# Kernel tuning notes

Measured on AMD Instinct MI355X. Metric: run time of the kernel, lower is better.

The kernel has to match this reference:

```python
import jax, jax.numpy as jnp
import numpy as np

N_NODES = 100000
N_EDGES = 1600000
IN_F, HID_F, OUT_F = 128, 128, 64


def setup_inputs() -> dict:
    key = jax.random.key(0)
    ks = jax.random.split(key, 8)
    x = jax.random.normal(ks[0], (N_NODES, IN_F), dtype=jnp.float32)
    edge_index = jax.random.randint(ks[1], (2, N_EDGES), 0, N_NODES, dtype=jnp.int64)
    w1 = jax.random.normal(ks[2], (IN_F, HID_F), dtype=jnp.float32) * 0.05
    b1 = jax.random.normal(ks[3], (HID_F,), dtype=jnp.float32) * 0.05
    c1 = jax.random.normal(ks[4], (IN_F, HID_F, 3), dtype=jnp.float32) * 0.01
    w2 = jax.random.normal(ks[5], (HID_F, OUT_F), dtype=jnp.float32) * 0.05
    b2 = jax.random.normal(ks[6], (OUT_F,), dtype=jnp.float32) * 0.05
    c2 = jax.random.normal(ks[7], (IN_F, OUT_F, 3), dtype=jnp.float32) * 0.01
    return {"x": x, "edge_index": edge_index, "w1": w1, "b1": b1, "c1": c1,
            "w2": w2, "b2": b2, "c2": c2}


def _minimal_kan(x, w, b, c):
    # linear term: (N, out)
    lin = x @ w + b
    # polynomial basis (x, x^2, x^3): (N, in, 3)
    basis = jnp.stack([x, x * x, x * x * x], axis=-1)
    # fused contraction over (in, 3); same math as the (N,in,out,3) broadcast-sum
    kan_out = jnp.einsum('nib,iob->no', basis, c)
    return lin + 0.1 * kan_out


def _aggregate(h, source, target, num_nodes):
    # mean over incoming messages, degree clamped at 1
    deg = jax.ops.segment_sum(jnp.ones(source.shape[0], dtype=h.dtype), target,
                              num_segments=num_nodes)
    deg = jnp.maximum(deg, 1.0)
    out = jax.ops.segment_sum(h[source], target, num_segments=num_nodes)
    return out / deg[:, None]


def reference(x, edge_index, w1, b1, c1, w2, b2, c2):
    source, target = edge_index[0], edge_index[1]
    n = x.shape[0]
    h = _minimal_kan(x, w1, b1, c1)
    h = jax.nn.relu(h)
    h = _aggregate(h, source, target, n)
    h = _minimal_kan(h, w2, b2, c2)
    h = _aggregate(h, source, target, n)
    return jax.nn.log_softmax(h, axis=-1)
```

## Files before the change

kernel.cpp:

```cpp
#include <hip/hip_runtime.h>
#include <hip/hip_bf16.h>
#include <math.h>

#define N_NODES 100000
#define N_EDGES 1600000
#define IN_F 128
#define HID_F 128
#define OUT_F 64
#define K_TOT 384
#define BST 392

#define BK_BITS 9
#define BK_SIZE 512
#define NBUCK ((N_NODES + BK_SIZE - 1) / BK_SIZE)
#define EPB 4096
#define NBLK_SORT ((N_EDGES + EPB - 1) / EPB)
#define BCAP 10240
#define PK_SRC_MASK 0x7fffffu
#define PAD8(d) (((d) + 7) & ~7)

typedef __attribute__((ext_vector_type(8))) short s8v;
typedef __attribute__((ext_vector_type(4))) short s4v;
typedef __attribute__((ext_vector_type(4))) float f4v;
typedef __attribute__((ext_vector_type(2))) float f2v;

__device__ __forceinline__ short f2bf(float f) {
    __hip_bfloat16 h = __float2bfloat16(f);
    return __builtin_bit_cast(short, h);
}

__global__ __launch_bounds__(256) void fold_weights_bf16(
    const float* __restrict__ w1, const float* __restrict__ c1,
    const float* __restrict__ w2, const float* __restrict__ c2,
    short* __restrict__ Wb1, short* __restrict__ Wb2,
    unsigned* __restrict__ h1d, unsigned* __restrict__ h2d)
{
    if (blockIdx.x == 0) {
        if (threadIdx.x < 32) h1d[(size_t)N_NODES * 32 + threadIdx.x] = 0;
        if (threadIdx.x < 16) h2d[(size_t)N_NODES * 16 + threadIdx.x] = 0;
    }
    int idx = blockIdx.x * 256 + threadIdx.x;
    if (idx < K_TOT * HID_F) {
        int k = idx >> 7, n = idx & 127;
        int p = k >> 7, f = k & 127;
        int si = f * HID_F + n;
        float v = (p == 0) ? (w1[si] + 0.1f * c1[si * 3])
                           : 0.1f * c1[si * 3 + p];
        Wb1[(((k >> 3) * HID_F) + n) * 8 + (k & 7)] = f2bf(v);
    } else {
        idx -= K_TOT * HID_F;
        if (idx < K_TOT * OUT_F) {
            int k = idx >> 6, n = idx & 63;
            int p = k >> 7, f = k & 127;
            int si = f * OUT_F + n;
            float v = (p == 0) ? (w2[si] + 0.1f * c2[si * 3])
                               : 0.1f * c2[si * 3 + p];
            Wb2[(((k >> 3) * OUT_F) + n) * 8 + (k & 7)] = f2bf(v);
        }
    }
}

__global__ __launch_bounds__(256) void bucket_init(int* __restrict__ bcur)
{
    int i = threadIdx.x;
    if (i < NBUCK) bcur[i] = i * BCAP;
}

__global__ __launch_bounds__(256) void bucket_scatter(
    const int* __restrict__ src, const int* __restrict__ tgt,
    int* __restrict__ bcur, unsigned* __restrict__ spk)
{
    __shared__ int h[NBUCK];
    __shared__ int base[NBUCK];
    int tid = threadIdx.x;
    for (int i = tid; i < NBUCK; i += 256) h[i] = 0;
    __syncthreads();
    int e0 = blockIdx.x * EPB;
    int n = min(EPB, N_EDGES - e0);
    for (int i = tid; i < n; i += 256)
        atomicAdd(&h[tgt[e0 + i] >> BK_BITS], 1);
    __syncthreads();
    for (int i = tid; i < NBUCK; i += 256) {
        int c = h[i];
        base[i] = c ? atomicAdd(&bcur[i], c) : 0;
        h[i] = 0;
    }
    __syncthreads();
    for (int i = tid; i < n; i += 256) {
        int t = tgt[e0 + i];
        int b = t >> BK_BITS;
        int pos = base[b] + atomicAdd(&h[b], 1);
        spk[pos] = ((unsigned)(t - (b << BK_BITS)) << 23) | (unsigned)src[e0 + i];
    }
}

__global__ __launch_bounds__(256) void bucket_degpad(
    const int* __restrict__ bcur, const unsigned* __restrict__ spk,
    int* __restrict__ deg, int* __restrict__ pbsum)
{
    __shared__ int d[BK_SIZE];
    __shared__ int s[256];
    int tid = threadIdx.x;
    int b = blockIdx.x;
    d[tid] = 0; d[tid + 256] = 0;
    __syncthreads();
    int e0 = b * BCAP, e1 = bcur[b];
    for (int i = e0 + tid; i < e1; i += 256)
        atomicAdd(&d[spk[i] >> 23], 1);
    __syncthreads();
    int nbase = b << BK_BITS;
    int a0 = d[2 * tid], a1c = d[2 * tid + 1];
    int n0 = nbase + 2 * tid, n1 = n0 + 1;
    if (n0 < N_NODES) deg[n0] = a0;
    if (n1 < N_NODES) deg[n1] = a1c;
    int pc0 = (n0 < N_NODES) ? PAD8(a0) : 0;
    int pc1 = (n1 < N_NODES) ? PAD8(a1c) : 0;
    s[tid] = pc0 + pc1;
    __syncthreads();
    for (int o = 128; o > 0; o >>= 1) {
        if (tid < o) s[tid] += s[tid + o];
        __syncthreads();
    }
    if (tid == 0) pbsum[b] = s[0];
}

__global__ __launch_bounds__(256) void csr_finalize(
    const int* __restrict__ bcur, const unsigned* __restrict__ spk,
    const int* __restrict__ deg, const int* __restrict__ pbsum,
    int* __restrict__ prow, int* __restrict__ csr_pad)
{
    __shared__ int s[256];
    __shared__ int cur[BK_SIZE];
    __shared__ int pst[BK_SIZE];
    int tid = threadIdx.x;
    int b = blockIdx.x;

    int v = (tid < NBUCK) ? pbsum[tid] : 0;
    s[tid] = v;
    __syncthreads();
    for (int o = 1; o < 256; o <<= 1) {
        int t = (tid >= o) ? s[tid - o] : 0;
        __syncthreads();
        s[tid] += t;
        __syncthreads();
    }
    int pboff_b = (b > 0) ? s[b - 1] : 0;
    int ptotal  = s[NBUCK - 1];
    __syncthreads();

    int nbase = b << BK_BITS;
    int n0 = nbase + 2 * tid, n1 = n0 + 1;
    int d0 = (n0 < N_NODES) ? deg[n0] : 0;
    int d1 = (n1 < N_NODES) ? deg[n1] : 0;
    int pc0 = (n0 < N_NODES) ? PAD8(d0) : 0;
    int pc1 = (n1 < N_NODES) ? PAD8(d1) : 0;
    int tsum = pc0 + pc1;
    s[tid] = tsum;
    __syncthreads();
    for (int o = 1; o < 256; o <<= 1) {
        int t = (tid >= o) ? s[tid - o] : 0;
        __syncthreads();
        s[tid] += t;
        __syncthreads();
    }
    int excl = s[tid] - tsum;
    int base = pboff_b + excl;
    if (n0 < N_NODES) { prow[n0] = base;       cur[2 * tid]     = base;       pst[2 * tid]     = base + pc0; }
    if (n1 < N_NODES) { prow[n1] = base + pc0; cur[2 * tid + 1] = base + pc0; pst[2 * tid + 1] = base + pc0 + pc1; }
    if (b == NBUCK - 1 && tid == 0) prow[N_NODES] = ptotal;
    __syncthreads();

    int e0 = b * BCAP, e1 = bcur[b];
    for (int i = e0 + tid; i < e1; i += 256) {
        unsigned pk = spk[i];
        int pos = atomicAdd(&cur[pk >> 23], 1);
        csr_pad[pos] = (int)(pk & PK_SRC_MASK);
    }
    __syncthreads();

    for (int i = tid; i < BK_SIZE; i += 256) {
        int nd = nbase + i;
        if (nd < N_NODES) {
            int kend = pst[i];
            for (int k = cur[i]; k < kend; ++k) csr_pad[k] = N_NODES;
        }
    }
}

__global__ __launch_bounds__(256) void kan1_mfma(
    const float* __restrict__ x, const short* __restrict__ Wb,
    const float* __restrict__ bias, unsigned* __restrict__ h1d)
{
    __shared__ short sb[64 * BST];
    const int tid  = threadIdx.x;
    const int lane = tid & 63;
    const int wave = tid >> 6;
    const int node0 = blockIdx.x * 64;
    const int q = lane >> 4, r = lane & 15;

#pragma unroll
    for (int it = 0; it < 8; ++it) {
        int idx = tid + 256 * it;
        int m = idx >> 5, c4 = (idx & 31) * 4;
        int gm = min(node0 + m, N_NODES - 1);
        float4 v = *(const float4*)(x + (size_t)gm * IN_F + c4);
        float vv[4] = {v.x, v.y, v.z, v.w};
        s4v p0, p1, p2;
#pragma unroll
        for (int t = 0; t < 4; ++t) {
            float e = vv[t], e2 = e * e, e3 = e2 * e;
            p0[t] = f2bf(e); p1[t] = f2bf(e2); p2[t] = f2bf(e3);
        }
        short* row = sb + m * BST + c4;
        *(s4v*)(row)       = p0;
        *(s4v*)(row + 128) = p1;
        *(s4v*)(row + 256) = p2;
    }
    __syncthreads();

    const int wm = (wave & 1) * 32;
    const int wn = (wave >> 1) * 64;

    f4v acc[2][4];
#pragma unroll
    for (int i = 0; i < 2; ++i)
#pragma unroll
        for (int j = 0; j < 4; ++j)
            acc[i][j] = (f4v){0.f, 0.f, 0.f, 0.f};

    float bj[4];
#pragma unroll
    for (int j = 0; j < 4; ++j) bj[j] = bias[wn + j * 16 + r];

#pragma unroll
    for (int kb = 0; kb < 12; ++kb) {
        const int col = kb * 32 + q * 8;
        s8v afrag[2];
#pragma unroll
        for (int i = 0; i < 2; ++i)
            afrag[i] = *(const s8v*)(sb + (wm + i * 16 + r) * BST + col);
#pragma unroll
        for (int j = 0; j < 4; ++j) {
            const s8v b = *(const s8v*)(Wb + (((kb * 4 + q) * HID_F) + wn + j * 16 + r) * 8);
            acc[0][j] = __builtin_amdgcn_mfma_f32_16x16x32_bf16(afrag[0], b, acc[0][j], 0, 0, 0);
            acc[1][j] = __builtin_amdgcn_mfma_f32_16x16x32_bf16(afrag[1], b, acc[1][j], 0, 0, 0);
        }
    }

    const int dci = ((wn >> 6) << 4) + r;
#pragma unroll
    for (int i = 0; i < 2; ++i)
#pragma unroll
        for (int e = 0; e < 4; ++e) {
            int grow = node0 + wm + i * 16 + q * 4 + e;
            if (grow < N_NODES) {
                float v0 = fmaxf(acc[i][0][e] + bj[0], 0.f);
                float v1 = fmaxf(acc[i][1][e] + bj[1], 0.f);
                float v2 = fmaxf(acc[i][2][e] + bj[2], 0.f);
                float v3 = fmaxf(acc[i][3][e] + bj[3], 0.f);
                int pk = __builtin_amdgcn_cvt_pk_fp8_f32(v0, v1, 0, false);
                pk = __builtin_amdgcn_cvt_pk_fp8_f32(v2, v3, pk, true);
                h1d[(size_t)grow * 32 + dci] = (unsigned)pk;
            }
        }
}

__global__ __launch_bounds__(256) void gather128(
    const unsigned* __restrict__ h1d, const int* __restrict__ prow,
    const int* __restrict__ csr_pad, unsigned* __restrict__ a1d)
{
    const int lane  = threadIdx.x & 63;
    const int wave  = threadIdx.x >> 6;
    const int hl    = lane & 31;
    const int half  = lane >> 5;
    const int hbase = half << 5;
    const int node  = blockIdx.x * 8 + wave * 2 + half;

    int p0 = prow[node], p1 = prow[node + 1];
    int cnt = p1 - p0;
    int cmax = max(cnt, __shfl_xor(cnt, 32));

    float acc[4][4];
#pragma unroll
    for (int t = 0; t < 4; ++t)
#pragma unroll
        for (int b = 0; b < 4; ++b) acc[t][b] = 0.f;

    for (int base = 0; base < cmax; base += 32) {
        int idx = max(min(p0 + base + hl, p1 - 1), 0);
        int sreg = csr_pad[idx];
        int lim = min(32, cmax - base);
        for (int j = 0; j < lim; j += 4) {
            if (base + j < cnt) {
                unsigned u[4];
#pragma unroll
                for (int t = 0; t < 4; ++t) {
                    int sj = __shfl(sreg, hbase + j + t);
                    u[t] = h1d[(size_t)sj * 32 + hl];
                }
#pragma unroll
                for (int t = 0; t < 4; ++t) {
                    f2v lo = __builtin_amdgcn_cvt_pk_f32_fp8(u[t], false);
                    f2v hi = __builtin_amdgcn_cvt_pk_f32_fp8(u[t], true);
                    acc[t][0] += lo.x; acc[t][1] += lo.y;
                    acc[t][2] += hi.x; acc[t][3] += hi.y;
                }
            }
        }
    }

    float s0 = (acc[0][0] + acc[1][0]) + (acc[2][0] + acc[3][0]);
    float s1 = (acc[0][1] + acc[1][1]) + (acc[2][1] + acc[3][1]);
    float s2 = (acc[0][2] + acc[1][2]) + (acc[2][2] + acc[3][2]);
    float s3 = (acc[0][3] + acc[1][3]) + (acc[2][3] + acc[3][3]);
    int pk = __builtin_amdgcn_cvt_pk_fp8_f32(s0, s1, 0, false);
    pk = __builtin_amdgcn_cvt_pk_fp8_f32(s2, s3, pk, true);
    a1d[(size_t)node * 32 + hl] = (unsigned)pk;
}

__global__ __launch_bounds__(256) void kan2_mfma(
    const unsigned* __restrict__ a1d, const int* __restrict__ deg,
    const short* __restrict__ Wb, const float* __restrict__ bias,
    unsigned short* __restrict__ h2s)
{
    __shared__ short sb[64 * BST];
    const int tid  = threadIdx.x;
    const int lane = tid & 63;
    const int wave = tid >> 6;
    const int node0 = blockIdx.x * 64;
    const int q = lane >> 4, r = lane & 15;

#pragma unroll
    for (int gi = 0; gi < 2; ++gi) {
        int g = tid + 256 * gi;
        int m = g >> 3, cg = (g & 7) * 4;
        int gm = min(node0 + m, N_NODES - 1);
        float di = 1.0f / fmaxf((float)deg[gm], 1.0f);
        uint4 u4 = *(const uint4*)(a1d + (size_t)gm * 32 + cg);
        unsigned uw[4] = {u4.x, u4.y, u4.z, u4.w};
        float xv[4][4];
#pragma unroll
        for (int j = 0; j < 4; ++j) {
            f2v lo = __builtin_amdgcn_cvt_pk_f32_fp8(uw[j], false);
            f2v hi = __builtin_amdgcn_cvt_pk_f32_fp8(uw[j], true);
            xv[j][0] = lo.x * di; xv[j][1] = lo.y * di;
            xv[j][2] = hi.x * di; xv[j][3] = hi.y * di;
        }
        int fb = ((cg >> 4) << 6) + (cg & 15);
#pragma unroll
        for (int b = 0; b < 4; ++b) {
            s4v p0, p1, p2;
#pragma unroll
            for (int j = 0; j < 4; ++j) {
                float e = xv[j][b], e2 = e * e, e3 = e2 * e;
                p0[j] = f2bf(e); p1[j] = f2bf(e2); p2[j] = f2bf(e3);
            }
            short* row = sb + m * BST + fb + 16 * b;
            *(s4v*)(row)       = p0;
            *(s4v*)(row + 128) = p1;
            *(s4v*)(row + 256) = p2;
        }
    }
    __syncthreads();

    const int wm = (wave & 1) * 32;
    const int wn = (wave >> 1) * 32;

    f4v acc[2][2];
#pragma unroll
    for (int i = 0; i < 2; ++i)
#pragma unroll
        for (int j = 0; j < 2; ++j)
            acc[i][j] = (f4v){0.f, 0.f, 0.f, 0.f};

    float bj[2];
#pragma unroll
    for (int j = 0; j < 2; ++j) bj[j] = bias[wn + j * 16 + r];

#pragma unroll
    for (int kb = 0; kb < 12; ++kb) {
        const int col = kb * 32 + q * 8;
        s8v afrag[2];
#pragma unroll
        for (int i = 0; i < 2; ++i)
            afrag[i] = *(const s8v*)(sb + (wm + i * 16 + r) * BST + col);
#pragma unroll
        for (int j = 0; j < 2; ++j) {
            const s8v b = *(const s8v*)(Wb + (((kb * 4 + q) * OUT_F) + wn + j * 16 + r) * 8);
            acc[0][j] = __builtin_amdgcn_mfma_f32_16x16x32_bf16(afrag[0], b, acc[0][j], 0, 0, 0);
            acc[1][j] = __builtin_amdgcn_mfma_f32_16x16x32_bf16(afrag[1], b, acc[1][j], 0, 0, 0);
        }
    }

    const int sslot = (wn >> 1) + r;
#pragma unroll
    for (int i = 0; i < 2; ++i)
#pragma unroll
        for (int e = 0; e < 4; ++e) {
            int grow = node0 + wm + i * 16 + q * 4 + e;
            if (grow < N_NODES) {
                float vlo = acc[i][0][e] + bj[0];
                float vhi = acc[i][1][e] + bj[1];
                int pk = __builtin_amdgcn_cvt_pk_fp8_f32(vlo, vhi, 0, false);
                h2s[(size_t)grow * 32 + sslot] = (unsigned short)(pk & 0xffff);
            }
        }
}

__global__ __launch_bounds__(256) void gather64_lsm(
    const unsigned short* __restrict__ h2s, const int* __restrict__ deg,
    const int* __restrict__ prow, const int* __restrict__ csr_pad,
    float* __restrict__ out)
{
    const int lane = threadIdx.x & 63;
    const int wave = threadIdx.x >> 6;
    const int hl   = lane & 31;
    const int half = lane >> 5;
    const int node = blockIdx.x * 8 + wave * 2 + half;

    int p0 = prow[node], p1 = prow[node + 1];
    int cnt = p1 - p0;
    int degr = deg[node];
    int cmax = max(cnt, __shfl_xor(cnt, 32));

    float alo[8], ahi[8];
#pragma unroll
    for (int t = 0; t < 8; ++t) { alo[t] = 0.f; ahi[t] = 0.f; }

    for (int base = 0; base < cmax; base += 32) {
        int idx = max(min(p0 + base + hl, p1 - 1), 0);
        int sreg = csr_pad[idx];
        int lim = min(32, cmax - base);
        for (int j = 0; j < lim; j += 8) {
            if (base + j < cnt) {
                int u[8];
#pragma unroll
                for (int t = 0; t < 8; ++t) {
                    int sj = __shfl(sreg, (half << 5) + j + t);
                    u[t] = (int)h2s[(size_t)sj * 32 + hl];
                }
#pragma unroll
                for (int t = 0; t < 8; ++t) {
                    alo[t] += __builtin_amdgcn_cvt_f32_fp8(u[t], 0);
                    ahi[t] += __builtin_amdgcn_cvt_f32_fp8(u[t], 1);
                }
            }
        }
    }
    float slo = ((alo[0] + alo[1]) + (alo[2] + alo[3])) + ((alo[4] + alo[5]) + (alo[6] + alo[7]));
    float shi = ((ahi[0] + ahi[1]) + (ahi[2] + ahi[3])) + ((ahi[4] + ahi[5]) + (ahi[6] + ahi[7]));

    float di = 1.0f / fmaxf((float)degr, 1.0f);
    float vlo = slo * di, vhi = shi * di;

    float m = fmaxf(vlo, vhi);
#pragma unroll
    for (int off = 16; off >= 1; off >>= 1)
        m = fmaxf(m, __shfl_xor(m, off));
    float e = expf(vlo - m) + expf(vhi - m);
#pragma unroll
    for (int off = 16; off >= 1; off >>= 1)
        e += __shfl_xor(e, off);
    float ls = logf(e);

    const int f_lo = ((hl >> 4) << 5) + (hl & 15);
    out[(size_t)node * OUT_F + f_lo]      = vlo - m - ls;
    out[(size_t)node * OUT_F + f_lo + 16] = vhi - m - ls;
}

extern "C" void kernel_launch(void* const* d_in, const int* in_sizes, int n_in,
                              void* d_out, int out_size, void* d_ws, size_t ws_size,
                              hipStream_t stream)
{
    const float* x  = (const float*)d_in[0];
    const int*   ei = (const int*)d_in[1];
    const float* w1 = (const float*)d_in[2];
    const float* b1 = (const float*)d_in[3];
    const float* c1 = (const float*)d_in[4];
    const float* w2 = (const float*)d_in[5];
    const float* b2 = (const float*)d_in[6];
    const float* c2 = (const float*)d_in[7];
    float* out = (float*)d_out;

    const int* src = ei;
    const int* tgt = ei + N_EDGES;

    char* ws = (char*)d_ws;
    size_t off = 0;
    auto carve = [&](size_t bytes) -> void* {
        void* p = ws + off;
        off = (off + bytes + 255) & ~(size_t)255;
        return p;
    };
    short*    Wb1       = (short*)carve((size_t)K_TOT * HID_F * 2);
    short*    Wb2       = (short*)carve((size_t)K_TOT * OUT_F * 2);
    int*      deg       = (int*)carve((size_t)N_NODES * 4);
    int*      prow      = (int*)carve(((size_t)N_NODES + 1) * 4);
    int*      bcur      = (int*)carve((size_t)NBUCK * 4);
    int*      pbsum     = (int*)carve((size_t)NBUCK * 4);
    unsigned* spk       = (unsigned*)carve((size_t)NBUCK * BCAP * 4);
    int*      csr_pad   = (int*)carve(((size_t)N_EDGES + 7 * (size_t)N_NODES + 64) * 4);
    unsigned* h1d       = (unsigned*)carve(((size_t)N_NODES + 1) * 128);
    unsigned* a1d       = (unsigned*)carve((size_t)N_NODES * 128);
    unsigned short* h2s = (unsigned short*)carve(((size_t)N_NODES + 1) * 64);

    const int grid_mm = (N_NODES + 63) / 64;

    bucket_init<<<1, 256, 0, stream>>>(bcur);
    bucket_scatter<<<NBLK_SORT, 256, 0, stream>>>(src, tgt, bcur, spk);
    bucket_degpad<<<NBUCK, 256, 0, stream>>>(bcur, spk, deg, pbsum);
    csr_finalize<<<NBUCK, 256, 0, stream>>>(bcur, spk, deg, pbsum, prow, csr_pad);

    fold_weights_bf16<<<(K_TOT * HID_F + K_TOT * OUT_F + 255) / 256, 256, 0, stream>>>(
        w1, c1, w2, c2, Wb1, Wb2, h1d, (unsigned*)h2s);
    kan1_mfma<<<grid_mm, 256, 0, stream>>>(x, Wb1, b1, h1d);

    gather128<<<(N_NODES + 7) / 8, 256, 0, stream>>>(h1d, prow, csr_pad, a1d);

    kan2_mfma<<<grid_mm, 256, 0, stream>>>(a1d, deg, Wb2, b2, h2s);

    gather64_lsm<<<(N_NODES + 7) / 8, 256, 0, stream>>>(
        h2s, deg, prow, csr_pad, out);
}
```

Baseline: 256.1 us.

## Merge CSR build kernels using fixed per-bucket padded capacity, drop global scan

Gives each target bucket a fixed-capacity region of the padded CSR array, so row offsets need only a local scan within the bucket. The degree/pad-sum kernel and the finalize kernel become one, and the cross-bucket prefix sum and pbsum array go away. The bucket counter init moves into the weight-folding kernel, and the scatter kernel keeps targets in shared memory instead of reading them twice. Gather kernels now take row length from the padded degree rather than prow[node+1]. The cost is a larger csr_pad allocation with gaps between buckets, and correctness now depends on no bucket exceeding BCAP edges.

```diff
diff --git a/kernel.cpp b/kernel.cpp
--- a/kernel.cpp
+++ b/kernel.cpp
@@ -16,6 +16,7 @@
 #define EPB 4096
 #define NBLK_SORT ((N_EDGES + EPB - 1) / EPB)
 #define BCAP 10240
+#define PCAP (BCAP + 7 * BK_SIZE)
 #define PK_SRC_MASK 0x7fffffu
 #define PAD8(d) (((d) + 7) & ~7)
 
@@ -33,11 +34,13 @@
     const float* __restrict__ w1, const float* __restrict__ c1,
     const float* __restrict__ w2, const float* __restrict__ c2,
     short* __restrict__ Wb1, short* __restrict__ Wb2,
-    unsigned* __restrict__ h1d, unsigned* __restrict__ h2d)
+    unsigned* __restrict__ h1d, unsigned* __restrict__ h2d,
+    int* __restrict__ bcur)
 {
     if (blockIdx.x == 0) {
         if (threadIdx.x < 32) h1d[(size_t)N_NODES * 32 + threadIdx.x] = 0;
         if (threadIdx.x < 16) h2d[(size_t)N_NODES * 16 + threadIdx.x] = 0;
+        if (threadIdx.x < NBUCK) bcur[threadIdx.x] = threadIdx.x * BCAP;
     }
     int idx = blockIdx.x * 256 + threadIdx.x;
     if (idx < K_TOT * HID_F) {
@@ -60,25 +63,23 @@
     }
 }
 
-__global__ __launch_bounds__(256) void bucket_init(int* __restrict__ bcur)
-{
-    int i = threadIdx.x;
-    if (i < NBUCK) bcur[i] = i * BCAP;
-}
-
 __global__ __launch_bounds__(256) void bucket_scatter(
     const int* __restrict__ src, const int* __restrict__ tgt,
     int* __restrict__ bcur, unsigned* __restrict__ spk)
 {
     __shared__ int h[NBUCK];
     __shared__ int base[NBUCK];
+    __shared__ int tg[EPB];
     int tid = threadIdx.x;
     for (int i = tid; i < NBUCK; i += 256) h[i] = 0;
     __syncthreads();
     int e0 = blockIdx.x * EPB;
     int n = min(EPB, N_EDGES - e0);
-    for (int i = tid; i < n; i += 256)
-        atomicAdd(&h[tgt[e0 + i] >> BK_BITS], 1);
+    for (int i = tid; i < n; i += 256) {
+        int t = tgt[e0 + i];
+        tg[i] = t;
+        atomicAdd(&h[t >> BK_BITS], 1);
+    }
     __syncthreads();
     for (int i = tid; i < NBUCK; i += 256) {
         int c = h[i];
@@ -87,18 +88,19 @@
     }
     __syncthreads();
     for (int i = tid; i < n; i += 256) {
-        int t = tgt[e0 + i];
+        int t = tg[i];
         int b = t >> BK_BITS;
         int pos = base[b] + atomicAdd(&h[b], 1);
         spk[pos] = ((unsigned)(t - (b << BK_BITS)) << 23) | (unsigned)src[e0 + i];
     }
 }
 
-__global__ __launch_bounds__(256) void bucket_degpad(
+__global__ __launch_bounds__(256) void csr_build(
     const int* __restrict__ bcur, const unsigned* __restrict__ spk,
-    int* __restrict__ deg, int* __restrict__ pbsum)
+    int* __restrict__ deg, int* __restrict__ prow, int* __restrict__ csr_pad)
 {
     __shared__ int d[BK_SIZE];
+    __shared__ int pst[BK_SIZE];
     __shared__ int s[256];
     int tid = threadIdx.x;
     int b = blockIdx.x;
@@ -115,28 +117,8 @@
     if (n1 < N_NODES) deg[n1] = a1c;
     int pc0 = (n0 < N_NODES) ? PAD8(a0) : 0;
     int pc1 = (n1 < N_NODES) ? PAD8(a1c) : 0;
-    s[tid] = pc0 + pc1;
-    __syncthreads();
-    for (int o = 128; o > 0; o >>= 1) {
-        if (tid < o) s[tid] += s[tid + o];
-        __syncthreads();
-    }
-    if (tid == 0) pbsum[b] = s[0];
-}
-
-__global__ __launch_bounds__(256) void csr_finalize(
-    const int* __restrict__ bcur, const unsigned* __restrict__ spk,
-    const int* __restrict__ deg, const int* __restrict__ pbsum,
-    int* __restrict__ prow, int* __restrict__ csr_pad)
-{
-    __shared__ int s[256];
-    __shared__ int cur[BK_SIZE];
-    __shared__ int pst[BK_SIZE];
-    int tid = threadIdx.x;
-    int b = blockIdx.x;
-
-    int v = (tid < NBUCK) ? pbsum[tid] : 0;
-    s[tid] = v;
+    int tsum = pc0 + pc1;
+    s[tid] = tsum;
     __syncthreads();
     for (int o = 1; o < 256; o <<= 1) {
         int t = (tid >= o) ? s[tid - o] : 0;
@@ -144,45 +126,25 @@
         s[tid] += t;
         __syncthreads();
     }
-    int pboff_b = (b > 0) ? s[b - 1] : 0;
-    int ptotal  = s[NBUCK - 1];
-    __syncthreads();
-
-    int nbase = b << BK_BITS;
-    int n0 = nbase + 2 * tid, n1 = n0 + 1;
-    int d0 = (n0 < N_NODES) ? deg[n0] : 0;
-    int d1 = (n1 < N_NODES) ? deg[n1] : 0;
-    int pc0 = (n0 < N_NODES) ? PAD8(d0) : 0;
-    int pc1 = (n1 < N_NODES) ? PAD8(d1) : 0;
-    int tsum = pc0 + pc1;
-    s[tid] = tsum;
-    __syncthreads();
-    for (int o = 1; o < 256; o <<= 1) {
-        int t = (tid >= o) ? s[tid - o] : 0;
-        __syncthreads();
-        s[tid] += t;
-        __syncthreads();
-    }
     int excl = s[tid] - tsum;
-    int base = pboff_b + excl;
-    if (n0 < N_NODES) { prow[n0] = base;       cur[2 * tid]     = base;       pst[2 * tid]     = base + pc0; }
-    if (n1 < N_NODES) { prow[n1] = base + pc0; cur[2 * tid + 1] = base + pc0; pst[2 * tid + 1] = base + pc0 + pc1; }
-    if (b == NBUCK - 1 && tid == 0) prow[N_NODES] = ptotal;
-    __syncthreads();
-
-    int e0 = b * BCAP, e1 = bcur[b];
+    int base = b * PCAP + excl;
+    if (n0 < N_NODES) prow[n0] = base;
+    if (n1 < N_NODES) prow[n1] = base + pc0;
+    __syncthreads();
+    d[2 * tid] = base;         pst[2 * tid]     = base + pc0;
+    d[2 * tid + 1] = base + pc0; pst[2 * tid + 1] = base + pc0 + pc1;
+    __syncthreads();
     for (int i = e0 + tid; i < e1; i += 256) {
         unsigned pk = spk[i];
-        int pos = atomicAdd(&cur[pk >> 23], 1);
+        int pos = atomicAdd(&d[pk >> 23], 1);
         csr_pad[pos] = (int)(pk & PK_SRC_MASK);
     }
     __syncthreads();
-
     for (int i = tid; i < BK_SIZE; i += 256) {
         int nd = nbase + i;
         if (nd < N_NODES) {
             int kend = pst[i];
-            for (int k = cur[i]; k < kend; ++k) csr_pad[k] = N_NODES;
+            for (int k = d[i]; k < kend; ++k) csr_pad[k] = N_NODES;
         }
     }
 }
@@ -267,7 +229,8 @@
 
 __global__ __launch_bounds__(256) void gather128(
     const unsigned* __restrict__ h1d, const int* __restrict__ prow,
-    const int* __restrict__ csr_pad, unsigned* __restrict__ a1d)
+    const int* __restrict__ deg, const int* __restrict__ csr_pad,
+    unsigned* __restrict__ a1d)
 {
     const int lane  = threadIdx.x & 63;
     const int wave  = threadIdx.x >> 6;
@@ -276,8 +239,9 @@
     const int hbase = half << 5;
     const int node  = blockIdx.x * 8 + wave * 2 + half;
 
-    int p0 = prow[node], p1 = prow[node + 1];
-    int cnt = p1 - p0;
+    int p0 = prow[node];
+    int cnt = PAD8(deg[node]);
+    int p1 = p0 + cnt;
     int cmax = max(cnt, __shfl_xor(cnt, 32));
 
     float acc[4][4];
@@ -418,9 +382,10 @@
     const int half = lane >> 5;
     const int node = blockIdx.x * 8 + wave * 2 + half;
 
-    int p0 = prow[node], p1 = prow[node + 1];
-    int cnt = p1 - p0;
+    int p0 = prow[node];
     int degr = deg[node];
+    int cnt = PAD8(degr);
+    int p1 = p0 + cnt;
     int cmax = max(cnt, __shfl_xor(cnt, 32));
 
     float alo[8], ahi[8];
@@ -495,27 +460,25 @@
     short*    Wb1       = (short*)carve((size_t)K_TOT * HID_F * 2);
     short*    Wb2       = (short*)carve((size_t)K_TOT * OUT_F * 2);
     int*      deg       = (int*)carve((size_t)N_NODES * 4);
-    int*      prow      = (int*)carve(((size_t)N_NODES + 1) * 4);
+    int*      prow      = (int*)carve((size_t)N_NODES * 4);
     int*      bcur      = (int*)carve((size_t)NBUCK * 4);
-    int*      pbsum     = (int*)carve((size_t)NBUCK * 4);
     unsigned* spk       = (unsigned*)carve((size_t)NBUCK * BCAP * 4);
-    int*      csr_pad   = (int*)carve(((size_t)N_EDGES + 7 * (size_t)N_NODES + 64) * 4);
+    int*      csr_pad   = (int*)carve((size_t)NBUCK * PCAP * 4);
     unsigned* h1d       = (unsigned*)carve(((size_t)N_NODES + 1) * 128);
     unsigned* a1d       = (unsigned*)carve((size_t)N_NODES * 128);
     unsigned short* h2s = (unsigned short*)carve(((size_t)N_NODES + 1) * 64);
 
     const int grid_mm = (N_NODES + 63) / 64;
 
-    bucket_init<<<1, 256, 0, stream>>>(bcur);
+    fold_weights_bf16<<<(K_TOT * HID_F + K_TOT * OUT_F + 255) / 256, 256, 0, stream>>>(
+        w1, c1, w2, c2, Wb1, Wb2, h1d, (unsigned*)h2s, bcur);
+
     bucket_scatter<<<NBLK_SORT, 256, 0, stream>>>(src, tgt, bcur, spk);
-    bucket_degpad<<<NBUCK, 256, 0, stream>>>(bcur, spk, deg, pbsum);
-    csr_finalize<<<NBUCK, 256, 0, stream>>>(bcur, spk, deg, pbsum, prow, csr_pad);
-
-    fold_weights_bf16<<<(K_TOT * HID_F + K_TOT * OUT_F + 255) / 256, 256, 0, stream>>>(
-        w1, c1, w2, c2, Wb1, Wb2, h1d, (unsigned*)h2s);
+    csr_build<<<NBUCK, 256, 0, stream>>>(bcur, spk, deg, prow, csr_pad);
+
     kan1_mfma<<<grid_mm, 256, 0, stream>>>(x, Wb1, b1, h1d);
 
-    gather128<<<(N_NODES + 7) / 8, 256, 0, stream>>>(h1d, prow, csr_pad, a1d);
+    gather128<<<(N_NODES + 7) / 8, 256, 0, stream>>>(h1d, prow, deg, csr_pad, a1d);
 
     kan2_mfma<<<grid_mm, 256, 0, stream>>>(a1d, deg, Wb2, b2, h2s);
 
```

Result: faster. 249.2 us (-2.7%).
